# Optimization experiments

Hardware: AMD Instinct MI355X
Metric: run time of the kernel (lower is better)

The kernel has to match this reference:

```python
import jax, jax.numpy as jnp
import numpy as np

B, L, D_IN, D_EDGE, H, D = 2, 384, 256, 128, 8, 32
SCALE = D ** (-0.5)


def setup_inputs() -> dict:
    key = jax.random.key(0)
    ks = jax.random.split(key, 12)
    hd = H * D
    s_in = D_IN ** -0.5
    s_e = D_EDGE ** -0.5
    return {
        "node_feat": jax.random.normal(ks[0], (B, L, D_IN), jnp.float32),
        "edge_feat": jax.random.normal(ks[1], (B, L, L, D_EDGE), jnp.float32),
        "edge_mask": (jax.random.uniform(ks[2], (B, L, L)) > 0.15).astype(jnp.float32),
        "Wq": jax.random.normal(ks[3], (D_IN, hd), jnp.float32) * s_in,
        "bq": jnp.zeros((hd,), jnp.float32),
        "Wk": jax.random.normal(ks[4], (D_IN, hd), jnp.float32) * s_in,
        "bk": jnp.zeros((hd,), jnp.float32),
        "Wv": jax.random.normal(ks[5], (D_IN, hd), jnp.float32) * s_in,
        "bv": jnp.zeros((hd,), jnp.float32),
        "We": jax.random.normal(ks[6], (D_EDGE, hd), jnp.float32) * s_e,
        "Wu": jax.random.normal(ks[7], (D_IN, hd), jnp.float32) * s_in,
        "bu": jnp.zeros((hd,), jnp.float32),
    }


def _split_heads(t):
    # (b, l, h*d) -> (b, h, l, d)
    b, l, _ = t.shape
    return t.reshape(b, l, H, D).transpose(0, 2, 1, 3)


def reference(node_feat, edge_feat, edge_mask, Wq, bq, Wk, bk, Wv, bv, We, Wu, bu):
    q = _split_heads(node_feat @ Wq + bq)
    k = _split_heads(node_feat @ Wk + bk)
    v = _split_heads(node_feat @ Wv + bv)
    # edge embedding: (b, i, j, h*d) -> (b, h, i, j, d)
    b, l = edge_feat.shape[0], edge_feat.shape[1]
    e = (edge_feat @ We).reshape(b, l, l, H, D).transpose(0, 3, 1, 2, 4)
    logit = jnp.einsum('bhid,bhjd->bhij', q, k)
    logit = logit + jnp.einsum('bhid,bhijd->bhij', q, e)
    att = logit * SCALE
    att = att + ((1.0 - edge_mask) * -1e9)[:, None, :, :]
    att = jax.nn.softmax(att, axis=-1)  # dropout is identity in eval / p=0
    updated = jnp.einsum('bhij,bhjd->bhid', att, v)
    updated = updated + jnp.einsum('bhij,bhijd->bhid', att, e)
    updated = updated.transpose(0, 2, 1, 3).reshape(b, l, H * D)
    return (node_feat @ Wu + bu) + updated
```

## Files before the change

kernel.cpp:

```cpp
#include <hip/hip_runtime.h>
#include <cstdint>

#define NB 2
#define LL 384
#define DIN 256
#define DE 128
#define NH 8
#define DH 32
#define HD 256
#define SCALE 0.17677669529663687f

typedef __attribute__((ext_vector_type(8))) short bf16x8;
typedef __attribute__((ext_vector_type(4))) float f32x4;

static __device__ __forceinline__ unsigned short f2bf(float f) {
    uint32_t u = __builtin_bit_cast(uint32_t, f);
    u += 0x7FFF + ((u >> 16) & 1);
    return (unsigned short)(u >> 16);
}
static __device__ __forceinline__ float bf2f(unsigned short u) {
    return __builtin_bit_cast(float, (uint32_t)u << 16);
}
static __device__ __forceinline__ float getf4(const float4& v, int k) {
    return k == 0 ? v.x : k == 1 ? v.y : k == 2 ? v.z : v.w;
}
static __device__ __forceinline__ bf16x8 pack8(const float4& a, const float4& b) {
    bf16x8 p;
    p[0]=(short)f2bf(a.x); p[1]=(short)f2bf(a.y); p[2]=(short)f2bf(a.z); p[3]=(short)f2bf(a.w);
    p[4]=(short)f2bf(b.x); p[5]=(short)f2bf(b.y); p[6]=(short)f2bf(b.z); p[7]=(short)f2bf(b.w);
    return p;
}

__global__ __launch_bounds__(128) void prep_we(const float* __restrict__ We,
                                               unsigned short* __restrict__ WeT) {
    const int n = blockIdx.x;
    const int k = threadIdx.x;
    WeT[n * DE + k] = f2bf(We[(size_t)k * HD + n]);
}

__global__ __launch_bounds__(256) void proj_kernel(
    const float* __restrict__ node,
    const float* __restrict__ Wq, const float* __restrict__ bq,
    const float* __restrict__ Wk, const float* __restrict__ bk,
    const float* __restrict__ Wv, const float* __restrict__ bv,
    const float* __restrict__ Wu, const float* __restrict__ bu,
    unsigned short* __restrict__ qb16, unsigned short* __restrict__ kb16,
    float* __restrict__ vb, float* __restrict__ ub)
{
    __shared__ __align__(16) float rows[4][DIN];
    const int t  = threadIdx.x;
    const int r0 = blockIdx.x * 4;

    #pragma unroll
    for (int r = 0; r < 4; ++r)
        rows[r][t] = node[(size_t)(r0 + r) * DIN + t];
    __syncthreads();

    float aq[4], ak[4], av[4], au[4];
    {
        const float vq = bq[t], vk = bk[t], vv = bv[t], vu = bu[t];
        #pragma unroll
        for (int r = 0; r < 4; ++r) { aq[r] = vq; ak[r] = vk; av[r] = vv; au[r] = vu; }
    }

    for (int f4 = 0; f4 < DIN / 4; ++f4) {
        float4 xv[4];
        #pragma unroll
        for (int r = 0; r < 4; ++r)
            xv[r] = *(const float4*)&rows[r][f4 * 4];
        #pragma unroll
        for (int k = 0; k < 4; ++k) {
            const int f = f4 * 4 + k;
            const float wq = Wq[(size_t)f * HD + t];
            const float wk = Wk[(size_t)f * HD + t];
            const float wv = Wv[(size_t)f * HD + t];
            const float wu = Wu[(size_t)f * HD + t];
            #pragma unroll
            for (int r = 0; r < 4; ++r) {
                const float x = getf4(xv[r], k);
                aq[r] += x * wq; ak[r] += x * wk; av[r] += x * wv; au[r] += x * wu;
            }
        }
    }

    #pragma unroll
    for (int r = 0; r < 4; ++r) {
        const size_t o = (size_t)(r0 + r) * HD + t;
        qb16[o] = f2bf(aq[r]); kb16[o] = f2bf(ak[r]);
        vb[o] = av[r]; ub[o] = au[r];
    }
}

__global__ __launch_bounds__(256) void vt_kernel(const float* __restrict__ vb,
                                                 unsigned short* __restrict__ vT) {
    __shared__ float tile[64][65];
    int blk = blockIdx.x;
    const int b  = blk / 24; blk %= 24;
    const int jt = blk / 4;
    const int ct = blk % 4;
    const int j0 = jt * 64, c0 = ct * 64;
    const int t  = threadIdx.x;
    const int c  = t & 63, j4 = t >> 6;
    #pragma unroll
    for (int rr = 0; rr < 16; ++rr) {
        const int j = j4 + 4 * rr;
        tile[j][c] = vb[(size_t)(b * LL + j0 + j) * HD + c0 + c];
    }
    __syncthreads();
    const int jj = t & 63, c4 = t >> 6;
    #pragma unroll
    for (int rr = 0; rr < 16; ++rr) {
        const int cc = c4 + 4 * rr;
        vT[(size_t)(b * HD + c0 + cc) * LL + j0 + jj] = f2bf(tile[jj][cc]);
    }
}

__global__ __launch_bounds__(256) void qk_kernel(
    const unsigned short* __restrict__ qb16, const unsigned short* __restrict__ kb16,
    const float* __restrict__ mask, float* __restrict__ logit_pre)
{
    int idx = blockIdx.x;
    const int jt = idx % 6; idx /= 6;
    const int it = idx % 6; idx /= 6;
    const int h  = idx % NH;
    const int b  = idx / NH;
    const int t    = threadIdx.x;
    const int lane = t & 63;
    const int w    = t >> 6;
    const int lid  = lane & 15;
    const int g    = lane >> 4;
    const int i0 = it * 64 + w * 16;
    const int j0 = jt * 64;

    const bf16x8 afr = *(const bf16x8*)&qb16[(size_t)(b * LL + i0 + lid) * HD + h * DH + g * 8];
    f32x4 acc[4];
    #pragma unroll
    for (int jj = 0; jj < 4; ++jj) {
        const bf16x8 bfrg = *(const bf16x8*)&kb16[(size_t)(b * LL + j0 + jj * 16 + lid) * HD + h * DH + g * 8];
        acc[jj] = __builtin_amdgcn_mfma_f32_16x16x32_bf16(afr, bfrg, (f32x4){0.f,0.f,0.f,0.f}, 0, 0, 0);
    }
    #pragma unroll
    for (int jj = 0; jj < 4; ++jj) {
        #pragma unroll
        for (int r = 0; r < 4; ++r) {
            const int i = i0 + 4 * g + r;
            const int j = j0 + jj * 16 + lid;
            const float lg = SCALE * acc[jj][r]
                           + (1.0f - mask[(size_t)(b * LL + i) * LL + j]) * -1e9f;
            logit_pre[((size_t)(b * NH + h) * LL + i) * LL + j] = lg;
        }
    }
}

__global__ __launch_bounds__(256) void qwe_kernel(
    const unsigned short* __restrict__ qb16, const unsigned short* __restrict__ WeT,
    unsigned short* __restrict__ qWe)
{
    const int bi = blockIdx.x;
    const int t  = threadIdx.x;
    const int h  = t >> 5;
    const int c0 = (t & 31) * 4;

    float qv[32];
    const unsigned short* qp = &qb16[(size_t)bi * HD + h * DH];
    #pragma unroll
    for (int d = 0; d < 32; ++d) qv[d] = bf2f(qp[d]);

    float acc0 = 0.f, acc1 = 0.f, acc2 = 0.f, acc3 = 0.f;
    #pragma unroll
    for (int d = 0; d < 32; ++d) {
        const ushort4 wt = *(const ushort4*)&WeT[(size_t)(h * DH + d) * DE + c0];
        acc0 += qv[d] * bf2f(wt.x); acc1 += qv[d] * bf2f(wt.y);
        acc2 += qv[d] * bf2f(wt.z); acc3 += qv[d] * bf2f(wt.w);
    }
    unsigned short* o = &qWe[(size_t)bi * (NH * DE) + h * DE + c0];
    o[0] = f2bf(SCALE * acc0); o[1] = f2bf(SCALE * acc1);
    o[2] = f2bf(SCALE * acc2); o[3] = f2bf(SCALE * acc3);
}

__global__ __launch_bounds__(512, 4) void att_kernel(
    const float* __restrict__ edge,
    const unsigned short* __restrict__ qWe,
    float* __restrict__ lpre)
{
    __shared__ float red0[64], red1[64];
    const int t = threadIdx.x, lane = t & 63, w = t >> 6;
    const int lid = lane & 15, g = lane >> 4;
    const int bi = blockIdx.x, b = bi / LL, ii = bi % LL;
    const int J  = w * 48;
    const int hq = lid & 7;

    bf16x8 bfr[4];
    const unsigned short* qwp = &qWe[(size_t)bi * (NH * DE) + hq * DE];
    #pragma unroll
    for (int kt = 0; kt < 4; ++kt)
        bfr[kt] = *(const bf16x8*)&qwp[kt * 32 + g * 8];

    f32x4 acc[3];
    #pragma unroll
    for (int mt = 0; mt < 3; ++mt) {
        acc[mt] = (f32x4){0.f, 0.f, 0.f, 0.f};
        const float* ef = edge + ((size_t)bi * LL + J + mt * 16 + lid) * DE;
        #pragma unroll
        for (int kt = 0; kt < 4; ++kt) {
            const float4 x0 = *(const float4*)&ef[kt * 32 + g * 8];
            const float4 x1 = *(const float4*)&ef[kt * 32 + g * 8 + 4];
            acc[mt] = __builtin_amdgcn_mfma_f32_16x16x32_bf16(pack8(x0, x1), bfr[kt], acc[mt], 0, 0, 0);
        }
    }

    float lg[12];
    float* lrow = lpre + ((size_t)(b * NH + hq) * LL + ii) * LL;
    #pragma unroll
    for (int mt = 0; mt < 3; ++mt)
        #pragma unroll
        for (int r = 0; r < 4; ++r) {
            const int j = J + mt * 16 + g * 4 + r;
            lg[mt * 4 + r] = (lid < 8) ? (acc[mt][r] + lrow[j]) : -3e38f;
        }

    float m = lg[0];
    #pragma unroll
    for (int k = 1; k < 12; ++k) m = fmaxf(m, lg[k]);
    m = fmaxf(m, __shfl_xor(m, 16));
    m = fmaxf(m, __shfl_xor(m, 32));
    if (lane < 8) red0[w * 8 + lane] = m;
    __syncthreads();
    float M = red0[hq];
    #pragma unroll
    for (int k = 1; k < 8; ++k) M = fmaxf(M, red0[k * 8 + hq]);

    float p[12], s = 0.f;
    #pragma unroll
    for (int k = 0; k < 12; ++k) { p[k] = __expf(lg[k] - M); s += p[k]; }
    s += __shfl_xor(s, 16); s += __shfl_xor(s, 32);
    if (lane < 8) red1[w * 8 + lane] = s;
    __syncthreads();
    float S = 0.f;
    #pragma unroll
    for (int k = 0; k < 8; ++k) S += red1[k * 8 + hq];
    const float inv = 1.0f / S;

    if (lid < 8) {
        #pragma unroll
        for (int mt = 0; mt < 3; ++mt)
            #pragma unroll
            for (int r = 0; r < 4; ++r)
                lrow[J + mt * 16 + g * 4 + r] = p[mt * 4 + r] * inv;
    }
}

#define TJ 64
#define NT (LL / TJ)
__global__ __launch_bounds__(512, 4) void pv_kernel(
    const float* __restrict__ edge,
    const float* __restrict__ att,
    const unsigned short* __restrict__ vT,
    const unsigned short* __restrict__ WeT,
    const float* __restrict__ ub,
    float* __restrict__ out)
{
    __shared__ __align__(16) unsigned short Es[2][TJ * DE];
    __shared__ __align__(16) unsigned short atts[NH * LL];
    __shared__ float smA[NH * DE];
    __shared__ float avs[HD];

    const int t = threadIdx.x, lane = t & 63, w = t >> 6;
    const int lid = lane & 15, g = lane >> 4;
    const int bi = blockIdx.x, b = bi / LL, ii = bi % LL;
    const float* efbase = edge + (size_t)bi * LL * DE;

    {
        const float* ar = att + ((size_t)(b * NH + w) * LL + ii) * LL;
        #pragma unroll
        for (int k = 0; k < 3; ++k) {
            const int j2 = (lane + 64 * k) * 2;
            const float2 x = *(const float2*)&ar[j2];
            const unsigned int pk = ((unsigned int)f2bf(x.y) << 16) | (unsigned int)f2bf(x.x);
            *(unsigned int*)&atts[w * LL + j2] = pk;
        }
    }
    #pragma unroll
    for (int q = 0; q < 2; ++q) {
        const int id = t + q * 512, sr = id >> 4, ci = id & 15;
        const float* src = efbase + (size_t)sr * DE + ci * 8;
        const float4 x0 = ((const float4*)src)[0], x1 = ((const float4*)src)[1];
        *(bf16x8*)&Es[0][sr * DE + ci * 8] = pack8(x0, x1);
    }
    __syncthreads();

    f32x4 accE = (f32x4){0.f, 0.f, 0.f, 0.f};
    f32x4 accV[2];
    accV[0] = (f32x4){0.f, 0.f, 0.f, 0.f};
    accV[1] = (f32x4){0.f, 0.f, 0.f, 0.f};

    for (int tile = 0; tile < NT; ++tile) {
        const int j0  = tile * TJ;
        const int cur = tile & 1;
        const unsigned short* Ecur = Es[cur];
        const bool have_next = (tile + 1 < NT);
        float4 nx[2][2];
        if (have_next) {
            #pragma unroll
            for (int q = 0; q < 2; ++q) {
                const int id = t + q * 512, sr = id >> 4, ci = id & 15;
                const float* src = efbase + (size_t)(j0 + TJ + sr) * DE + ci * 8;
                nx[q][0] = ((const float4*)src)[0];
                nx[q][1] = ((const float4*)src)[1];
            }
        }
        #pragma unroll
        for (int kt = 0; kt < 2; ++kt) {
            const int jb = j0 + kt * 32;
            const bf16x8 bf = *(const bf16x8*)&atts[(lid & 7) * LL + jb + g * 8];
            bf16x8 ae;
            #pragma unroll
            for (int u = 0; u < 8; ++u)
                ae[u] = (short)Ecur[(kt * 32 + g * 8 + u) * DE + 16 * w + lid];
            accE = __builtin_amdgcn_mfma_f32_16x16x32_bf16(ae, bf, accE, 0, 0, 0);
            #pragma unroll
            for (int mt = 0; mt < 2; ++mt) {
                const bf16x8 va = *(const bf16x8*)&vT[(size_t)(b * HD + w * DH + mt * 16 + lid) * LL + jb + g * 8];
                accV[mt] = __builtin_amdgcn_mfma_f32_16x16x32_bf16(va, bf, accV[mt], 0, 0, 0);
            }
        }
        if (have_next) {
            #pragma unroll
            for (int q = 0; q < 2; ++q) {
                const int id = t + q * 512, sr = id >> 4, ci = id & 15;
                *(bf16x8*)&Es[cur ^ 1][sr * DE + ci * 8] = pack8(nx[q][0], nx[q][1]);
            }
        }
        __syncthreads();
    }

    if (lid < 8) {
        #pragma unroll
        for (int r = 0; r < 4; ++r)
            smA[lid * DE + 16 * w + 4 * g + r] = accE[r];
    }
    if (lid == w) {
        #pragma unroll
        for (int mt = 0; mt < 2; ++mt)
            #pragma unroll
            for (int r = 0; r < 4; ++r)
                avs[w * DH + mt * 16 + 4 * g + r] = accV[mt][r];
    }
    __syncthreads();

    if (lane < 32) {
        const int hd = w * DH + lane;
        float o = ub[(size_t)bi * HD + hd] + avs[hd];
        const unsigned short* wrow = &WeT[(size_t)hd * DE];
        const float* sa = &smA[w * DE];
        #pragma unroll
        for (int c = 0; c < DE; c += 4) {
            const ushort4 wt = *(const ushort4*)&wrow[c];
            o += sa[c]     * bf2f(wt.x);
            o += sa[c + 1] * bf2f(wt.y);
            o += sa[c + 2] * bf2f(wt.z);
            o += sa[c + 3] * bf2f(wt.w);
        }
        out[(size_t)bi * HD + hd] = o;
    }
}

extern "C" void kernel_launch(void* const* d_in, const int* in_sizes, int n_in,
                              void* d_out, int out_size, void* d_ws, size_t ws_size,
                              hipStream_t stream) {
    const float* node = (const float*)d_in[0];
    const float* edge = (const float*)d_in[1];
    const float* mask = (const float*)d_in[2];
    const float* Wq   = (const float*)d_in[3];
    const float* bq   = (const float*)d_in[4];
    const float* Wk   = (const float*)d_in[5];
    const float* bk   = (const float*)d_in[6];
    const float* Wv   = (const float*)d_in[7];
    const float* bv   = (const float*)d_in[8];
    const float* We   = (const float*)d_in[9];
    const float* Wu   = (const float*)d_in[10];
    const float* bu   = (const float*)d_in[11];
    float* out = (float*)d_out;

    const size_t rowsz = (size_t)NB * LL * HD;
    float* ws   = (float*)d_ws;
    float* vb   = ws;
    float* ubuf = vb + rowsz;
    float* lpre = ubuf + rowsz;
    unsigned short* us   = (unsigned short*)(lpre + (size_t)NB * NH * LL * LL);
    unsigned short* WeT  = us;
    unsigned short* qb16 = WeT + (size_t)HD * DE;
    unsigned short* kb16 = qb16 + rowsz;
    unsigned short* vT   = kb16 + rowsz;
    unsigned short* qWeB = vT + rowsz;

    hipLaunchKernelGGL(prep_we, dim3(HD), dim3(DE), 0, stream, We, WeT);
    hipLaunchKernelGGL(proj_kernel, dim3(NB * LL / 4), dim3(256), 0, stream,
                       node, Wq, bq, Wk, bk, Wv, bv, Wu, bu, qb16, kb16, vb, ubuf);
    hipLaunchKernelGGL(vt_kernel, dim3(NB * (LL / 64) * (HD / 64)), dim3(256), 0, stream,
                       vb, vT);
    hipLaunchKernelGGL(qk_kernel, dim3(NB * NH * (LL / 64) * (LL / 64)), dim3(256), 0, stream,
                       qb16, kb16, mask, lpre);
    hipLaunchKernelGGL(qwe_kernel, dim3(NB * LL), dim3(256), 0, stream,
                       qb16, WeT, qWeB);
    hipLaunchKernelGGL(att_kernel, dim3(NB * LL), dim3(512), 0, stream,
                       edge, qWeB, lpre);
    hipLaunchKernelGGL(pv_kernel, dim3(NB * LL), dim3(512), 0, stream,
                       edge, lpre, vT, WeT, ubuf, out);
}
```

Measured before the change: 118.7 us.

## Split attention and PV stages into finer-grained kernels with j-tile parallelism

The fused edge-logit+softmax kernel is split into an edge-logit kernel over three j-tiles per row and a separate row-wise softmax kernel that writes bf16 probabilities. The PV kernel is also split across three j-tiles, writing partial attention-edge and attention-value sums to workspace, and a new finale kernel reduces them and applies We. This raises grid parallelism from 768 blocks to 2304 and drops the shared-memory double-buffer loop. In exchange it adds two kernel launches and extra global round-trips for logits and partial sums.

```diff
diff --git a/kernel.cpp b/kernel.cpp
--- a/kernel.cpp
+++ b/kernel.cpp
@@ -178,17 +178,19 @@
     o[2] = f2bf(SCALE * acc2); o[3] = f2bf(SCALE * acc3);
 }
 
-__global__ __launch_bounds__(512, 4) void att_kernel(
+__global__ __launch_bounds__(256) void elog_kernel(
     const float* __restrict__ edge,
     const unsigned short* __restrict__ qWe,
     float* __restrict__ lpre)
 {
-    __shared__ float red0[64], red1[64];
+    int idx = blockIdx.x;
+    const int jt = idx % 3; idx /= 3;
+    const int bi = idx;
+    const int b = bi / LL, ii = bi % LL;
     const int t = threadIdx.x, lane = t & 63, w = t >> 6;
     const int lid = lane & 15, g = lane >> 4;
-    const int bi = blockIdx.x, b = bi / LL, ii = bi % LL;
-    const int J  = w * 48;
     const int hq = lid & 7;
+    const int j0 = jt * 128 + w * 32;
 
     bf16x8 bfr[4];
     const unsigned short* qwp = &qWe[(size_t)bi * (NH * DE) + hq * DE];
@@ -196,11 +198,11 @@
     for (int kt = 0; kt < 4; ++kt)
         bfr[kt] = *(const bf16x8*)&qwp[kt * 32 + g * 8];
 
-    f32x4 acc[3];
-    #pragma unroll
-    for (int mt = 0; mt < 3; ++mt) {
+    f32x4 acc[2];
+    #pragma unroll
+    for (int mt = 0; mt < 2; ++mt) {
         acc[mt] = (f32x4){0.f, 0.f, 0.f, 0.f};
-        const float* ef = edge + ((size_t)bi * LL + J + mt * 16 + lid) * DE;
+        const float* ef = edge + ((size_t)bi * LL + j0 + mt * 16 + lid) * DE;
         #pragma unroll
         for (int kt = 0; kt < 4; ++kt) {
             const float4 x0 = *(const float4*)&ef[kt * 32 + g * 8];
@@ -209,160 +211,151 @@
         }
     }
 
-    float lg[12];
-    float* lrow = lpre + ((size_t)(b * NH + hq) * LL + ii) * LL;
-    #pragma unroll
-    for (int mt = 0; mt < 3; ++mt)
-        #pragma unroll
-        for (int r = 0; r < 4; ++r) {
-            const int j = J + mt * 16 + g * 4 + r;
-            lg[mt * 4 + r] = (lid < 8) ? (acc[mt][r] + lrow[j]) : -3e38f;
+    if (lid < 8) {
+        float* lrow = lpre + ((size_t)(b * NH + hq) * LL + ii) * LL;
+        #pragma unroll
+        for (int mt = 0; mt < 2; ++mt) {
+            float4* p4 = (float4*)&lrow[j0 + mt * 16 + 4 * g];
+            float4 x = *p4;
+            x.x += acc[mt][0]; x.y += acc[mt][1];
+            x.z += acc[mt][2]; x.w += acc[mt][3];
+            *p4 = x;
         }
-
-    float m = lg[0];
-    #pragma unroll
-    for (int k = 1; k < 12; ++k) m = fmaxf(m, lg[k]);
-    m = fmaxf(m, __shfl_xor(m, 16));
-    m = fmaxf(m, __shfl_xor(m, 32));
-    if (lane < 8) red0[w * 8 + lane] = m;
-    __syncthreads();
-    float M = red0[hq];
-    #pragma unroll
-    for (int k = 1; k < 8; ++k) M = fmaxf(M, red0[k * 8 + hq]);
-
-    float p[12], s = 0.f;
-    #pragma unroll
-    for (int k = 0; k < 12; ++k) { p[k] = __expf(lg[k] - M); s += p[k]; }
-    s += __shfl_xor(s, 16); s += __shfl_xor(s, 32);
-    if (lane < 8) red1[w * 8 + lane] = s;
-    __syncthreads();
-    float S = 0.f;
-    #pragma unroll
-    for (int k = 0; k < 8; ++k) S += red1[k * 8 + hq];
-    const float inv = 1.0f / S;
-
-    if (lid < 8) {
-        #pragma unroll
-        for (int mt = 0; mt < 3; ++mt)
-            #pragma unroll
-            for (int r = 0; r < 4; ++r)
-                lrow[J + mt * 16 + g * 4 + r] = p[mt * 4 + r] * inv;
-    }
-}
-
-#define TJ 64
-#define NT (LL / TJ)
-__global__ __launch_bounds__(512, 4) void pv_kernel(
+    }
+}
+
+__global__ __launch_bounds__(256) void smax_kernel(
+    const float* __restrict__ lpre, unsigned short* __restrict__ attb)
+{
+    const int t = threadIdx.x, lane = t & 63, w = t >> 6;
+    const int row = blockIdx.x * 4 + w;
+    const float* lr = lpre + (size_t)row * LL;
+
+    float2 x[3];
+    #pragma unroll
+    for (int k = 0; k < 3; ++k)
+        x[k] = *(const float2*)&lr[2 * lane + 128 * k];
+
+    float m = fmaxf(x[0].x, x[0].y);
+    m = fmaxf(m, fmaxf(x[1].x, x[1].y));
+    m = fmaxf(m, fmaxf(x[2].x, x[2].y));
+    #pragma unroll
+    for (int off = 1; off < 64; off <<= 1) m = fmaxf(m, __shfl_xor(m, off));
+
+    float p[6], s = 0.f;
+    #pragma unroll
+    for (int k = 0; k < 3; ++k) {
+        p[2 * k]     = __expf(x[k].x - m);
+        p[2 * k + 1] = __expf(x[k].y - m);
+        s += p[2 * k] + p[2 * k + 1];
+    }
+    #pragma unroll
+    for (int off = 1; off < 64; off <<= 1) s += __shfl_xor(s, off);
+    const float inv = 1.0f / s;
+
+    unsigned int* ao = (unsigned int*)attb + (size_t)row * (LL / 2);
+    #pragma unroll
+    for (int k = 0; k < 3; ++k) {
+        const unsigned int pk = ((unsigned int)f2bf(p[2 * k + 1] * inv) << 16)
+                              |  (unsigned int)f2bf(p[2 * k] * inv);
+        ao[lane + 64 * k] = pk;
+    }
+}
+
+__global__ __launch_bounds__(512, 4) void pvs_kernel(
     const float* __restrict__ edge,
-    const float* __restrict__ att,
+    const unsigned short* __restrict__ attb,
     const unsigned short* __restrict__ vT,
-    const unsigned short* __restrict__ WeT,
-    const float* __restrict__ ub,
-    float* __restrict__ out)
-{
-    __shared__ __align__(16) unsigned short Es[2][TJ * DE];
-    __shared__ __align__(16) unsigned short atts[NH * LL];
-    __shared__ float smA[NH * DE];
-    __shared__ float avs[HD];
-
+    float* __restrict__ aEp,
+    float* __restrict__ avp)
+{
+    int idx = blockIdx.x;
+    const int jt = idx % 3; idx /= 3;
+    const int bi = idx;
+    const int b = bi / LL, ii = bi % LL;
     const int t = threadIdx.x, lane = t & 63, w = t >> 6;
     const int lid = lane & 15, g = lane >> 4;
-    const int bi = blockIdx.x, b = bi / LL, ii = bi % LL;
-    const float* efbase = edge + (size_t)bi * LL * DE;
-
-    {
-        const float* ar = att + ((size_t)(b * NH + w) * LL + ii) * LL;
-        #pragma unroll
-        for (int k = 0; k < 3; ++k) {
-            const int j2 = (lane + 64 * k) * 2;
-            const float2 x = *(const float2*)&ar[j2];
-            const unsigned int pk = ((unsigned int)f2bf(x.y) << 16) | (unsigned int)f2bf(x.x);
-            *(unsigned int*)&atts[w * LL + j2] = pk;
-        }
-    }
-    #pragma unroll
-    for (int q = 0; q < 2; ++q) {
-        const int id = t + q * 512, sr = id >> 4, ci = id & 15;
-        const float* src = efbase + (size_t)sr * DE + ci * 8;
-        const float4 x0 = ((const float4*)src)[0], x1 = ((const float4*)src)[1];
-        *(bf16x8*)&Es[0][sr * DE + ci * 8] = pack8(x0, x1);
-    }
-    __syncthreads();
-
+    const int h = lid & 7;
+    const int j0 = jt * 128;
+
+    bf16x8 pA[4];
+    const unsigned short* ab = attb + ((size_t)(b * NH + h) * LL + ii) * LL + j0;
+    #pragma unroll
+    for (int kt = 0; kt < 4; ++kt)
+        pA[kt] = *(const bf16x8*)&ab[kt * 32 + g * 8];
+
+    const float* Eb = edge + ((size_t)bi * LL + j0) * DE + w * 16 + lid;
     f32x4 accE = (f32x4){0.f, 0.f, 0.f, 0.f};
+    #pragma unroll
+    for (int kt = 0; kt < 4; ++kt) {
+        bf16x8 be;
+        #pragma unroll
+        for (int u = 0; u < 8; ++u)
+            be[u] = (short)f2bf(Eb[(size_t)(kt * 32 + g * 8 + u) * DE]);
+        accE = __builtin_amdgcn_mfma_f32_16x16x32_bf16(pA[kt], be, accE, 0, 0, 0);
+    }
+
     f32x4 accV[2];
     accV[0] = (f32x4){0.f, 0.f, 0.f, 0.f};
     accV[1] = (f32x4){0.f, 0.f, 0.f, 0.f};
-
-    for (int tile = 0; tile < NT; ++tile) {
-        const int j0  = tile * TJ;
-        const int cur = tile & 1;
-        const unsigned short* Ecur = Es[cur];
-        const bool have_next = (tile + 1 < NT);
-        float4 nx[2][2];
-        if (have_next) {
-            #pragma unroll
-            for (int q = 0; q < 2; ++q) {
-                const int id = t + q * 512, sr = id >> 4, ci = id & 15;
-                const float* src = efbase + (size_t)(j0 + TJ + sr) * DE + ci * 8;
-                nx[q][0] = ((const float4*)src)[0];
-                nx[q][1] = ((const float4*)src)[1];
-            }
+    #pragma unroll
+    for (int kt = 0; kt < 4; ++kt) {
+        #pragma unroll
+        for (int mt = 0; mt < 2; ++mt) {
+            const bf16x8 vv = *(const bf16x8*)&vT[(size_t)(b * HD + w * DH + mt * 16 + lid) * LL + j0 + kt * 32 + g * 8];
+            accV[mt] = __builtin_amdgcn_mfma_f32_16x16x32_bf16(pA[kt], vv, accV[mt], 0, 0, 0);
         }
-        #pragma unroll
-        for (int kt = 0; kt < 2; ++kt) {
-            const int jb = j0 + kt * 32;
-            const bf16x8 bf = *(const bf16x8*)&atts[(lid & 7) * LL + jb + g * 8];
-            bf16x8 ae;
-            #pragma unroll
-            for (int u = 0; u < 8; ++u)
-                ae[u] = (short)Ecur[(kt * 32 + g * 8 + u) * DE + 16 * w + lid];
-            accE = __builtin_amdgcn_mfma_f32_16x16x32_bf16(ae, bf, accE, 0, 0, 0);
-            #pragma unroll
-            for (int mt = 0; mt < 2; ++mt) {
-                const bf16x8 va = *(const bf16x8*)&vT[(size_t)(b * HD + w * DH + mt * 16 + lid) * LL + jb + g * 8];
-                accV[mt] = __builtin_amdgcn_mfma_f32_16x16x32_bf16(va, bf, accV[mt], 0, 0, 0);
-            }
-        }
-        if (have_next) {
-            #pragma unroll
-            for (int q = 0; q < 2; ++q) {
-                const int id = t + q * 512, sr = id >> 4, ci = id & 15;
-                *(bf16x8*)&Es[cur ^ 1][sr * DE + ci * 8] = pack8(nx[q][0], nx[q][1]);
-            }
-        }
-        __syncthreads();
-    }
-
-    if (lid < 8) {
+    }
+
+    float* aep = aEp + (size_t)(bi * 3 + jt) * (NH * DE);
+    if (g < 2) {
         #pragma unroll
         for (int r = 0; r < 4; ++r)
-            smA[lid * DE + 16 * w + 4 * g + r] = accE[r];
-    }
-    if (lid == w) {
-        #pragma unroll
-        for (int mt = 0; mt < 2; ++mt)
-            #pragma unroll
-            for (int r = 0; r < 4; ++r)
-                avs[w * DH + mt * 16 + 4 * g + r] = accV[mt][r];
+            aep[(4 * g + r) * DE + w * 16 + lid] = accE[r];
+    }
+    float* avo = avp + (size_t)(bi * 3 + jt) * HD;
+    #pragma unroll
+    for (int mt = 0; mt < 2; ++mt)
+        #pragma unroll
+        for (int r = 0; r < 4; ++r)
+            if (4 * g + r == w)
+                avo[w * DH + mt * 16 + lid] = accV[mt][r];
+}
+
+__global__ __launch_bounds__(256) void finale_kernel(
+    const float* __restrict__ aEp, const float* __restrict__ avp,
+    const float* __restrict__ We,
+    const float* __restrict__ ub,
+    float* __restrict__ out)
+{
+    __shared__ float aEs[NH * DE];
+    const int bi = blockIdx.x, t = threadIdx.x;
+
+    #pragma unroll
+    for (int q = 0; q < 4; ++q) {
+        const int x = t + 256 * q;
+        aEs[x] = aEp[(size_t)(bi * 3 + 0) * (NH * DE) + x]
+               + aEp[(size_t)(bi * 3 + 1) * (NH * DE) + x]
+               + aEp[(size_t)(bi * 3 + 2) * (NH * DE) + x];
     }
     __syncthreads();
 
-    if (lane < 32) {
-        const int hd = w * DH + lane;
-        float o = ub[(size_t)bi * HD + hd] + avs[hd];
-        const unsigned short* wrow = &WeT[(size_t)hd * DE];
-        const float* sa = &smA[w * DE];
-        #pragma unroll
-        for (int c = 0; c < DE; c += 4) {
-            const ushort4 wt = *(const ushort4*)&wrow[c];
-            o += sa[c]     * bf2f(wt.x);
-            o += sa[c + 1] * bf2f(wt.y);
-            o += sa[c + 2] * bf2f(wt.z);
-            o += sa[c + 3] * bf2f(wt.w);
-        }
-        out[(size_t)bi * HD + hd] = o;
-    }
+    const int hd = t, h = hd >> 5;
+    float acc = ub[(size_t)bi * HD + hd]
+              + avp[(size_t)(bi * 3 + 0) * HD + hd]
+              + avp[(size_t)(bi * 3 + 1) * HD + hd]
+              + avp[(size_t)(bi * 3 + 2) * HD + hd];
+
+    const float* sa = &aEs[h * DE];
+    float a0 = 0.f, a1 = 0.f, a2 = 0.f, a3 = 0.f;
+    #pragma unroll
+    for (int c = 0; c < DE; c += 4) {
+        a0 += sa[c]     * We[(size_t)(c)     * HD + hd];
+        a1 += sa[c + 1] * We[(size_t)(c + 1) * HD + hd];
+        a2 += sa[c + 2] * We[(size_t)(c + 2) * HD + hd];
+        a3 += sa[c + 3] * We[(size_t)(c + 3) * HD + hd];
+    }
+    out[(size_t)bi * HD + hd] = acc + ((a0 + a1) + (a2 + a3));
 }
 
 extern "C" void kernel_launch(void* const* d_in, const int* in_sizes, int n_in,
@@ -383,16 +376,20 @@
     float* out = (float*)d_out;
 
     const size_t rowsz = (size_t)NB * LL * HD;
+    const size_t lsz   = (size_t)NB * NH * LL * LL;
     float* ws   = (float*)d_ws;
     float* vb   = ws;
     float* ubuf = vb + rowsz;
     float* lpre = ubuf + rowsz;
-    unsigned short* us   = (unsigned short*)(lpre + (size_t)NB * NH * LL * LL);
+    float* aEp  = lpre + lsz;
+    float* avp  = aEp + (size_t)NB * LL * 3 * NH * DE;
+    unsigned short* us   = (unsigned short*)(avp + (size_t)NB * LL * 3 * HD);
     unsigned short* WeT  = us;
     unsigned short* qb16 = WeT + (size_t)HD * DE;
     unsigned short* kb16 = qb16 + rowsz;
     unsigned short* vT   = kb16 + rowsz;
     unsigned short* qWeB = vT + rowsz;
+    unsigned short* attb = qWeB + (size_t)NB * LL * NH * DE;
 
     hipLaunchKernelGGL(prep_we, dim3(HD), dim3(DE), 0, stream, We, WeT);
     hipLaunchKernelGGL(proj_kernel, dim3(NB * LL / 4), dim3(256), 0, stream,
@@ -403,8 +400,12 @@
                        qb16, kb16, mask, lpre);
     hipLaunchKernelGGL(qwe_kernel, dim3(NB * LL), dim3(256), 0, stream,
                        qb16, WeT, qWeB);
-    hipLaunchKernelGGL(att_kernel, dim3(NB * LL), dim3(512), 0, stream,
+    hipLaunchKernelGGL(elog_kernel, dim3(NB * LL * 3), dim3(256), 0, stream,
                        edge, qWeB, lpre);
-    hipLaunchKernelGGL(pv_kernel, dim3(NB * LL), dim3(512), 0, stream,
-                       edge, lpre, vT, WeT, ubuf, out);
-}
+    hipLaunchKernelGGL(smax_kernel, dim3(NB * NH * LL / 4), dim3(256), 0, stream,
+                       lpre, attb);
+    hipLaunchKernelGGL(pvs_kernel, dim3(NB * LL * 3), dim3(512), 0, stream,
+                       edge, attb, vT, aEp, avp);
+    hipLaunchKernelGGL(finale_kernel, dim3(NB * LL), dim3(256), 0, stream,
+                       aEp, avp, We, ubuf, out);
+}
```

New measurement: 121.9 us. +2.7%, slower.

## Fuse softmax and attention-value/edge aggregation into one flash-style kernel

Applied to the files above, without the earlier changes.

Merges att_kernel and pv_kernel into a single kernel. Each wave computes a local softmax over its 48-column slice and keeps unnormalized probabilities in LDS. It then computes partial att·E and att·V products and merges them across waves with max/sum rescaling, like flash attention. This removes the write and re-read of the normalized attention matrix and the second full pass over edge_feat. The cost is uncoalesced strided gathers of edge elements for the B operand, extra LDS traffic, and a final We projection that reads fp32 We column-strided.

```diff
diff --git a/kernel.cpp b/kernel.cpp
--- a/kernel.cpp
+++ b/kernel.cpp
@@ -178,190 +178,167 @@
     o[2] = f2bf(SCALE * acc2); o[3] = f2bf(SCALE * acc3);
 }
 
-__global__ __launch_bounds__(512, 4) void att_kernel(
+__global__ __launch_bounds__(512, 4) void fused_kernel(
     const float* __restrict__ edge,
     const unsigned short* __restrict__ qWe,
-    float* __restrict__ lpre)
+    const float* __restrict__ lpre,
+    const unsigned short* __restrict__ vT,
+    const float* __restrict__ We,
+    const float* __restrict__ ub,
+    float* __restrict__ out)
 {
-    __shared__ float red0[64], red1[64];
+    __shared__ __align__(16) unsigned short p_lds[8 * 8 * 64];
+    __shared__ float aEw[8 * NH * DE];
+    __shared__ float avw[8 * HD];
+    __shared__ float mlw[8][2][NH];
+    __shared__ float aEm[NH * DE];
+
     const int t = threadIdx.x, lane = t & 63, w = t >> 6;
     const int lid = lane & 15, g = lane >> 4;
     const int bi = blockIdx.x, b = bi / LL, ii = bi % LL;
-    const int J  = w * 48;
-    const int hq = lid & 7;
-
-    bf16x8 bfr[4];
-    const unsigned short* qwp = &qWe[(size_t)bi * (NH * DE) + hq * DE];
-    #pragma unroll
-    for (int kt = 0; kt < 4; ++kt)
-        bfr[kt] = *(const bf16x8*)&qwp[kt * 32 + g * 8];
+    const int j0w = w * 48;
+    const int h8 = lid & 7;
+
+    bf16x8 qfr[4];
+    {
+        const unsigned short* qwp = &qWe[(size_t)bi * (NH * DE) + h8 * DE];
+        #pragma unroll
+        for (int kt = 0; kt < 4; ++kt)
+            qfr[kt] = *(const bf16x8*)&qwp[kt * 32 + g * 8];
+    }
 
     f32x4 acc[3];
     #pragma unroll
     for (int mt = 0; mt < 3; ++mt) {
         acc[mt] = (f32x4){0.f, 0.f, 0.f, 0.f};
-        const float* ef = edge + ((size_t)bi * LL + J + mt * 16 + lid) * DE;
+        const float* ef = edge + ((size_t)bi * LL + j0w + mt * 16 + lid) * DE;
         #pragma unroll
         for (int kt = 0; kt < 4; ++kt) {
             const float4 x0 = *(const float4*)&ef[kt * 32 + g * 8];
             const float4 x1 = *(const float4*)&ef[kt * 32 + g * 8 + 4];
-            acc[mt] = __builtin_amdgcn_mfma_f32_16x16x32_bf16(pack8(x0, x1), bfr[kt], acc[mt], 0, 0, 0);
-        }
-    }
-
+            acc[mt] = __builtin_amdgcn_mfma_f32_16x16x32_bf16(pack8(x0, x1), qfr[kt], acc[mt], 0, 0, 0);
+        }
+    }
+
+    const float* lrow = lpre + ((size_t)(b * NH + h8) * LL + ii) * LL;
     float lg[12];
-    float* lrow = lpre + ((size_t)(b * NH + hq) * LL + ii) * LL;
-    #pragma unroll
-    for (int mt = 0; mt < 3; ++mt)
-        #pragma unroll
-        for (int r = 0; r < 4; ++r) {
-            const int j = J + mt * 16 + g * 4 + r;
-            lg[mt * 4 + r] = (lid < 8) ? (acc[mt][r] + lrow[j]) : -3e38f;
-        }
+    #pragma unroll
+    for (int mt = 0; mt < 3; ++mt) {
+        const float4 qk4 = *(const float4*)&lrow[j0w + mt * 16 + 4 * g];
+        #pragma unroll
+        for (int r = 0; r < 4; ++r)
+            lg[mt * 4 + r] = (lid < 8) ? (acc[mt][r] + getf4(qk4, r)) : -3e38f;
+    }
 
     float m = lg[0];
     #pragma unroll
     for (int k = 1; k < 12; ++k) m = fmaxf(m, lg[k]);
     m = fmaxf(m, __shfl_xor(m, 16));
     m = fmaxf(m, __shfl_xor(m, 32));
-    if (lane < 8) red0[w * 8 + lane] = m;
-    __syncthreads();
-    float M = red0[hq];
-    #pragma unroll
-    for (int k = 1; k < 8; ++k) M = fmaxf(M, red0[k * 8 + hq]);
-
     float p[12], s = 0.f;
     #pragma unroll
-    for (int k = 0; k < 12; ++k) { p[k] = __expf(lg[k] - M); s += p[k]; }
+    for (int k = 0; k < 12; ++k) { p[k] = __expf(lg[k] - m); s += p[k]; }
     s += __shfl_xor(s, 16); s += __shfl_xor(s, 32);
-    if (lane < 8) red1[w * 8 + lane] = s;
-    __syncthreads();
-    float S = 0.f;
-    #pragma unroll
-    for (int k = 0; k < 8; ++k) S += red1[k * 8 + hq];
-    const float inv = 1.0f / S;
-
+    if (lane < 8) { mlw[w][0][lane] = m; mlw[w][1][lane] = s; }
+
+    unsigned short* pw = &p_lds[w * 512];
     if (lid < 8) {
         #pragma unroll
         for (int mt = 0; mt < 3; ++mt)
             #pragma unroll
             for (int r = 0; r < 4; ++r)
-                lrow[J + mt * 16 + g * 4 + r] = p[mt * 4 + r] * inv;
-    }
-}
-
-#define TJ 64
-#define NT (LL / TJ)
-__global__ __launch_bounds__(512, 4) void pv_kernel(
-    const float* __restrict__ edge,
-    const float* __restrict__ att,
-    const unsigned short* __restrict__ vT,
-    const unsigned short* __restrict__ WeT,
-    const float* __restrict__ ub,
-    float* __restrict__ out)
-{
-    __shared__ __align__(16) unsigned short Es[2][TJ * DE];
-    __shared__ __align__(16) unsigned short atts[NH * LL];
-    __shared__ float smA[NH * DE];
-    __shared__ float avs[HD];
-
-    const int t = threadIdx.x, lane = t & 63, w = t >> 6;
-    const int lid = lane & 15, g = lane >> 4;
-    const int bi = blockIdx.x, b = bi / LL, ii = bi % LL;
-    const float* efbase = edge + (size_t)bi * LL * DE;
+                pw[lid * 64 + mt * 16 + 4 * g + r] = f2bf(p[mt * 4 + r]);
+    }
+    ((unsigned int*)pw)[(lane >> 3) * 32 + 24 + (lane & 7)] = 0;
+
+    bf16x8 pA[2];
+    #pragma unroll
+    for (int kt = 0; kt < 2; ++kt)
+        pA[kt] = *(const bf16x8*)&pw[h8 * 64 + kt * 32 + g * 8];
 
     {
-        const float* ar = att + ((size_t)(b * NH + w) * LL + ii) * LL;
-        #pragma unroll
-        for (int k = 0; k < 3; ++k) {
-            const int j2 = (lane + 64 * k) * 2;
-            const float2 x = *(const float2*)&ar[j2];
-            const unsigned int pk = ((unsigned int)f2bf(x.y) << 16) | (unsigned int)f2bf(x.x);
-            *(unsigned int*)&atts[w * LL + j2] = pk;
-        }
-    }
+        float* aEp_w = &aEw[w * NH * DE];
+        #pragma unroll
+        for (int ct = 0; ct < 8; ++ct) {
+            f32x4 aacc = (f32x4){0.f, 0.f, 0.f, 0.f};
+            #pragma unroll
+            for (int kt = 0; kt < 2; ++kt) {
+                bf16x8 be;
+                #pragma unroll
+                for (int u = 0; u < 8; ++u) {
+                    int jj = j0w + kt * 32 + g * 8 + u;
+                    jj = jj > LL - 1 ? LL - 1 : jj;
+                    be[u] = (short)f2bf(edge[((size_t)bi * LL + jj) * DE + ct * 16 + lid]);
+                }
+                aacc = __builtin_amdgcn_mfma_f32_16x16x32_bf16(pA[kt], be, aacc, 0, 0, 0);
+            }
+            if (g < 2) {
+                #pragma unroll
+                for (int r = 0; r < 4; ++r)
+                    aEp_w[(4 * g + r) * DE + ct * 16 + lid] = aacc[r];
+            }
+        }
+    }
+
+    {
+        float* av_w = &avw[w * HD];
+        const unsigned short* vTb = vT + (size_t)b * HD * LL;
+        #pragma unroll
+        for (int nt = 0; nt < 16; ++nt) {
+            f32x4 vacc = (f32x4){0.f, 0.f, 0.f, 0.f};
+            #pragma unroll
+            for (int kt = 0; kt < 2; ++kt) {
+                const bf16x8 vv = *(const bf16x8*)&vTb[(size_t)(nt * 16 + lid) * LL + j0w + kt * 32 + g * 8];
+                vacc = __builtin_amdgcn_mfma_f32_16x16x32_bf16(pA[kt], vv, vacc, 0, 0, 0);
+            }
+            const int hn = nt >> 1;
+            if (g == (hn >> 2)) av_w[nt * 16 + lid] = vacc[hn & 3];
+        }
+    }
+
+    __syncthreads();
+
     #pragma unroll
     for (int q = 0; q < 2; ++q) {
-        const int id = t + q * 512, sr = id >> 4, ci = id & 15;
-        const float* src = efbase + (size_t)sr * DE + ci * 8;
-        const float4 x0 = ((const float4*)src)[0], x1 = ((const float4*)src)[1];
-        *(bf16x8*)&Es[0][sr * DE + ci * 8] = pack8(x0, x1);
+        const int idx = t + q * 512;
+        const int h = idx >> 7, c = idx & 127;
+        float M = mlw[0][0][h];
+        #pragma unroll
+        for (int w2 = 1; w2 < 8; ++w2) M = fmaxf(M, mlw[w2][0][h]);
+        float L = 0.f, a = 0.f;
+        #pragma unroll
+        for (int w2 = 0; w2 < 8; ++w2) {
+            const float f = __expf(mlw[w2][0][h] - M);
+            L += f * mlw[w2][1][h];
+            a += f * aEw[w2 * NH * DE + h * DE + c];
+        }
+        aEm[idx] = a / L;
     }
     __syncthreads();
 
-    f32x4 accE = (f32x4){0.f, 0.f, 0.f, 0.f};
-    f32x4 accV[2];
-    accV[0] = (f32x4){0.f, 0.f, 0.f, 0.f};
-    accV[1] = (f32x4){0.f, 0.f, 0.f, 0.f};
-
-    for (int tile = 0; tile < NT; ++tile) {
-        const int j0  = tile * TJ;
-        const int cur = tile & 1;
-        const unsigned short* Ecur = Es[cur];
-        const bool have_next = (tile + 1 < NT);
-        float4 nx[2][2];
-        if (have_next) {
-            #pragma unroll
-            for (int q = 0; q < 2; ++q) {
-                const int id = t + q * 512, sr = id >> 4, ci = id & 15;
-                const float* src = efbase + (size_t)(j0 + TJ + sr) * DE + ci * 8;
-                nx[q][0] = ((const float4*)src)[0];
-                nx[q][1] = ((const float4*)src)[1];
-            }
-        }
-        #pragma unroll
-        for (int kt = 0; kt < 2; ++kt) {
-            const int jb = j0 + kt * 32;
-            const bf16x8 bf = *(const bf16x8*)&atts[(lid & 7) * LL + jb + g * 8];
-            bf16x8 ae;
-            #pragma unroll
-            for (int u = 0; u < 8; ++u)
-                ae[u] = (short)Ecur[(kt * 32 + g * 8 + u) * DE + 16 * w + lid];
-            accE = __builtin_amdgcn_mfma_f32_16x16x32_bf16(ae, bf, accE, 0, 0, 0);
-            #pragma unroll
-            for (int mt = 0; mt < 2; ++mt) {
-                const bf16x8 va = *(const bf16x8*)&vT[(size_t)(b * HD + w * DH + mt * 16 + lid) * LL + jb + g * 8];
-                accV[mt] = __builtin_amdgcn_mfma_f32_16x16x32_bf16(va, bf, accV[mt], 0, 0, 0);
-            }
-        }
-        if (have_next) {
-            #pragma unroll
-            for (int q = 0; q < 2; ++q) {
-                const int id = t + q * 512, sr = id >> 4, ci = id & 15;
-                *(bf16x8*)&Es[cur ^ 1][sr * DE + ci * 8] = pack8(nx[q][0], nx[q][1]);
-            }
-        }
-        __syncthreads();
-    }
-
-    if (lid < 8) {
-        #pragma unroll
-        for (int r = 0; r < 4; ++r)
-            smA[lid * DE + 16 * w + 4 * g + r] = accE[r];
-    }
-    if (lid == w) {
-        #pragma unroll
-        for (int mt = 0; mt < 2; ++mt)
-            #pragma unroll
-            for (int r = 0; r < 4; ++r)
-                avs[w * DH + mt * 16 + 4 * g + r] = accV[mt][r];
-    }
-    __syncthreads();
-
-    if (lane < 32) {
-        const int hd = w * DH + lane;
-        float o = ub[(size_t)bi * HD + hd] + avs[hd];
-        const unsigned short* wrow = &WeT[(size_t)hd * DE];
-        const float* sa = &smA[w * DE];
+    if (t < HD) {
+        const int hd = t, h = hd >> 5;
+        float M = mlw[0][0][h];
+        #pragma unroll
+        for (int w2 = 1; w2 < 8; ++w2) M = fmaxf(M, mlw[w2][0][h]);
+        float L = 0.f, avv = 0.f;
+        #pragma unroll
+        for (int w2 = 0; w2 < 8; ++w2) {
+            const float f = __expf(mlw[w2][0][h] - M);
+            L += f * mlw[w2][1][h];
+            avv += f * avw[w2 * HD + hd];
+        }
+        float o = ub[(size_t)bi * HD + hd] + avv / L;
+        const float* sa = &aEm[h * DE];
+        float a0 = 0.f, a1 = 0.f, a2 = 0.f, a3 = 0.f;
         #pragma unroll
         for (int c = 0; c < DE; c += 4) {
-            const ushort4 wt = *(const ushort4*)&wrow[c];
-            o += sa[c]     * bf2f(wt.x);
-            o += sa[c + 1] * bf2f(wt.y);
-            o += sa[c + 2] * bf2f(wt.z);
-            o += sa[c + 3] * bf2f(wt.w);
-        }
-        out[(size_t)bi * HD + hd] = o;
+            a0 += sa[c]     * We[(size_t)(c)     * HD + hd];
+            a1 += sa[c + 1] * We[(size_t)(c + 1) * HD + hd];
+            a2 += sa[c + 2] * We[(size_t)(c + 2) * HD + hd];
+            a3 += sa[c + 3] * We[(size_t)(c + 3) * HD + hd];
+        }
+        out[(size_t)bi * HD + hd] = o + ((a0 + a1) + (a2 + a3));
     }
 }
 
@@ -383,11 +360,12 @@
     float* out = (float*)d_out;
 
     const size_t rowsz = (size_t)NB * LL * HD;
+    const size_t lsz   = (size_t)NB * NH * LL * LL;
     float* ws   = (float*)d_ws;
     float* vb   = ws;
     float* ubuf = vb + rowsz;
     float* lpre = ubuf + rowsz;
-    unsigned short* us   = (unsigned short*)(lpre + (size_t)NB * NH * LL * LL);
+    unsigned short* us   = (unsigned short*)(lpre + lsz);
     unsigned short* WeT  = us;
     unsigned short* qb16 = WeT + (size_t)HD * DE;
     unsigned short* kb16 = qb16 + rowsz;
@@ -403,8 +381,6 @@
                        qb16, kb16, mask, lpre);
     hipLaunchKernelGGL(qwe_kernel, dim3(NB * LL), dim3(256), 0, stream,
                        qb16, WeT, qWeB);
-    hipLaunchKernelGGL(att_kernel, dim3(NB * LL), dim3(512), 0, stream,
-                       edge, qWeB, lpre);
-    hipLaunchKernelGGL(pv_kernel, dim3(NB * LL), dim3(512), 0, stream,
-                       edge, lpre, vT, WeT, ubuf, out);
-}
+    hipLaunchKernelGGL(fused_kernel, dim3(NB * LL), dim3(512), 0, stream,
+                       edge, qWeB, lpre, vT, We, ubuf, out);
+}
```

Result: faster. 114.4 us (-3.6%).
